# Performance work log

Measured on AMD Instinct MI355X. Metric: run time of the kernel, lower is better.

## Reference

```python
import jax, jax.numpy as jnp
import numpy as np

PRIMES = [2, 3, 5, 7]  # from prime2idx {"2":0,"3":1,"5":2,"7":3}
NEG = float('-inf')


def setup_inputs() -> dict:
    B, O, T, P, L = 16384, 7, 64, 4, 7
    ks = jax.random.split(jax.random.key(0), 12)
    return {
        'program_seq': jax.random.randint(ks[0], (B, 20), 0, 7),
        'order_mask': jnp.zeros((B, O), jnp.float32),
        'tile_remain_budgets': jax.random.randint(ks[1], (B, L, P), 0, T),
        'tile_masks': jnp.zeros((B, L, P, T), jnp.float32),
        'cur_buffer_level': 1,
        'loop_ind': 2,
        'remain_buffer_size': jax.random.uniform(ks[2], (B,), jnp.float32, 1.0, 1e6),
        'tile2_max': jax.random.randint(ks[3], (B,), 32, T),
        'max_temporal_tile2': jax.random.uniform(ks[4], (B,), jnp.float32, 0.0, 10.0),
        'sp_tile2_max': jax.random.randint(ks[5], (B,), 16, 32),
        'sp_tile2_min': jax.random.randint(ks[6], (B,), 0, 8),
        'order_logit': jax.random.normal(ks[7], (B, O), jnp.float32),
        'tile_logits': jax.random.normal(ks[8], (B, P, T), jnp.float32),
        'sp_tile2_logit': jax.random.normal(ks[9], (B, T), jnp.float32),
    }


def _sample(key, score, mask):
    # categorical sample, its log-prob, and the 'more-than-one-option' mask
    action = jax.random.categorical(key, score)
    lp = jnp.take_along_axis(jax.nn.log_softmax(score, axis=-1), action[:, None], axis=1)[:, 0]
    lpm = ((mask == 0).sum(axis=-1) > 1).astype(score.dtype)
    return action, lp, lpm


def reference(program_seq, order_mask, tile_remain_budgets, tile_masks,
              cur_buffer_level, loop_ind, remain_buffer_size, tile2_max,
              max_temporal_tile2, sp_tile2_max, sp_tile2_min,
              order_logit, tile_logits, sp_tile2_logit):
    B = program_seq.shape[0]
    T = tile_masks.shape[-1]
    P = tile_logits.shape[1]
    n_levels = 3  # len(buffer_size_list)
    keys = jax.random.split(jax.random.key(1), 2 + P)
    j = jnp.arange(T)[None, :]  # [1,T] position grid for range masks

    # ---- order head ----
    order_score = order_logit + order_mask
    order_action, order_lp, order_lpm = _sample(keys[0], order_score, order_mask)

    if cur_buffer_level == n_levels:
        log_probs = jnp.zeros((B, 1 + P + 1), order_score.dtype).at[:, 0].set(order_lp)
        log_prob_masks = jnp.zeros((B, 1 + P + 1), order_score.dtype).at[:, 0].set(order_lpm)
        return order_action, None, None, log_probs, log_prob_masks

    tile2_base = tile_masks[:, loop_ind, 0]  # [B,T]

    # ---- spatial tile2: vectorized [min,max] range mask (replaces per-sample loops) ----
    sp_mask = jnp.where((j > sp_tile2_max[:, None]) | (j < sp_tile2_min[:, None]), NEG, tile2_base)
    sp_score = sp_tile2_logit + sp_mask
    sp_action, sp_lp, sp_lpm = _sample(keys[1], sp_score, sp_mask)

    # ---- temporal tile2 ----
    tile2_min = sp_action
    t2_max = jnp.minimum(tile2_max, tile2_min + max_temporal_tile2.astype(tile2_max.dtype))
    t2_mask = jnp.where((j > t2_max[:, None]) | (j < tile2_min[:, None]), NEG, tile2_base)
    t2_score = tile_logits[:, 0] + t2_mask
    tile2_action, t2_lp, t2_lpm = _sample(keys[2], t2_score, t2_mask)

    tile_actions = [tile2_action]
    sp_tile_actions = [sp_action]
    log_probs = [order_lp, t2_lp]
    log_prob_masks = [order_lpm, t2_lpm]

    tile_action = tile2_action
    rbs = remain_buffer_size
    for p in range(1, P):  # small fixed loop over primes
        rbs = rbs / jnp.power(jnp.float32(PRIMES[p - 1]), tile_action.astype(jnp.float32))
        tmax = jnp.log2(jnp.clip(rbs, 1.0)) / np.log2(PRIMES[p])
        tmax = jnp.clip(tmax.astype(jnp.int32), 0, T - 1)
        tmax = jnp.minimum(tmax, tile_remain_budgets[:, loop_ind, p].astype(jnp.int32))
        mask = jnp.where(j > tmax[:, None], NEG, tile_masks[:, loop_ind, p])
        score = tile_logits[:, p] + mask
        tile_action, lp, lpm = _sample(keys[2 + p], score, mask)
        tile_actions.append(tile_action)
        log_probs.append(lp)
        log_prob_masks.append(lpm)
        sp_tile_actions.append(jnp.zeros((B,), program_seq.dtype))

    log_probs.append(sp_lp)
    log_prob_masks.append(sp_lpm)

    return (order_action,
            jnp.stack(tile_actions, axis=1),
            jnp.stack(sp_tile_actions, axis=1),
            jnp.stack(log_probs, axis=1),
            jnp.stack(log_prob_masks, axis=1))
```

## Files before the change

kernel.cpp:

```cpp
#include <hip/hip_runtime.h>
#include <stdint.h>
#include <math.h>

__host__ __device__ static inline void tf2x32(uint32_t k0, uint32_t k1,
                                              uint32_t& x0, uint32_t& x1) {
  uint32_t ks2 = k0 ^ k1 ^ 0x1BD11BDAu;
  x0 += k0; x1 += k1;
#define TFR(r) { x0 += x1; x1 = (x1 << (r)) | (x1 >> (32 - (r))); x1 ^= x0; }
  TFR(13) TFR(15) TFR(26) TFR(6)
  x0 += k1;  x1 += ks2 + 1u;
  TFR(17) TFR(29) TFR(16) TFR(24)
  x0 += ks2; x1 += k0 + 2u;
  TFR(13) TFR(15) TFR(26) TFR(6)
  x0 += k0;  x1 += k1 + 3u;
  TFR(17) TFR(29) TFR(16) TFR(24)
  x0 += k1;  x1 += ks2 + 4u;
  TFR(13) TFR(15) TFR(26) TFR(6)
  x0 += ks2; x1 += k0 + 5u;
#undef TFR
}

struct Keys { uint32_t k[12]; };

struct SampleOut { int action; float lp; float lpm; };

__device__ static inline SampleOut wave_sample(uint32_t k0, uint32_t k1,
                                               uint32_t flat_idx, int n, int t,
                                               float score, float maskval) {
  const bool active = (t < n);
  const float NEGINF = -__builtin_inff();
  float sc = active ? score : NEGINF;

  uint32_t x0 = 0u, x1 = flat_idx;
  tf2x32(k0, k1, x0, x1);
  uint32_t bits = x0 ^ x1;
  uint32_t fb = (bits >> 9) | 0x3f800000u;
  float f = __uint_as_float(fb) - 1.0f;
  const float tinyf = 1.1754943508222875e-38f;
  float u = fmaxf(tinyf, f + tinyf);
  float g = -logf(-logf(u));

  float z  = active ? (sc + g) : NEGINF;
  float es = active ? expf(sc) : 0.0f;

  float zv = z; int zi = t;
#pragma unroll
  for (int m = 1; m < 64; m <<= 1) {
    float ov = __shfl_xor(zv, m, 64);
    int   oi = __shfl_xor(zi, m, 64);
    es += __shfl_xor(es, m, 64);
    bool take = (ov > zv) || (ov == zv && oi < zi);
    zv = take ? ov : zv;
    zi = take ? oi : zi;
  }
  int action = zi;

  float sa = __shfl(sc, action, 64);
  float lp = sa - logf(es);

  unsigned long long ball = __ballot(active && (maskval == 0.0f));
  SampleOut r;
  r.action = action;
  r.lp = lp;
  r.lpm = (__popcll(ball) > 1) ? 1.0f : 0.0f;
  return r;
}

__device__ static inline double ipow_d(int base, int e) {
  double r = 1.0, b = (double)base;
  while (e) { if (e & 1) r *= b; b *= b; e >>= 1; }
  return r;
}

__global__ __launch_bounds__(256) void pt_kernel(
    const int*   __restrict__ loop_ind_p,
    const float* __restrict__ order_mask,
    const int*   __restrict__ tile_remain_budgets,
    const float* __restrict__ tile_masks,
    const float* __restrict__ remain_buffer_size,
    const int*   __restrict__ tile2_max,
    const float* __restrict__ max_temporal_tile2,
    const int*   __restrict__ sp_tile2_max,
    const int*   __restrict__ sp_tile2_min,
    const float* __restrict__ order_logit,
    const float* __restrict__ tile_logits,
    const float* __restrict__ sp_tile2_logit,
    float*       __restrict__ out,
    int B, int O, int T, int P, int L, Keys keys) {
  const int wave = threadIdx.x >> 6;
  const int t    = threadIdx.x & 63;
  const int b    = blockIdx.x * (blockDim.x >> 6) + wave;
  if (b >= B) return;

  const float NEGINF = -__builtin_inff();
  const int li = loop_ind_p[0];

  float om = (t < O) ? order_mask[(size_t)b * O + t] : 1.0f;
  float osc = (t < O) ? (order_logit[(size_t)b * O + t] + om) : NEGINF;
  SampleOut so = wave_sample(keys.k[0], keys.k[1],
                             (uint32_t)(b * O + t), O, t, osc, om);

  const float* tm_row = tile_masks + ((size_t)b * L + li) * P * T;
  float t2base = tm_row[t];
  int spmx = sp_tile2_max[b], spmn = sp_tile2_min[b];
  float spmask = (t > spmx || t < spmn) ? NEGINF : t2base;
  float spsc = sp_tile2_logit[(size_t)b * T + t] + spmask;
  SampleOut ssp = wave_sample(keys.k[2], keys.k[3],
                              (uint32_t)(b * T + t), T, t, spsc, spmask);

  int t2min = ssp.action;
  int mt = (int)max_temporal_tile2[b];
  int t2mx = min(tile2_max[b], t2min + mt);
  float t2mask = (t > t2mx || t < t2min) ? NEGINF : t2base;
  float t2sc = tile_logits[(size_t)b * P * T + t] + t2mask;
  SampleOut st2 = wave_sample(keys.k[4], keys.k[5],
                              (uint32_t)(b * T + t), T, t, t2sc, t2mask);

  const float L2P[4] = {1.0f, 1.5849625007211562f, 2.321928094887362f,
                        2.807354922057604f};
  const int PRIMES_[4] = {2, 3, 5, 7};
  int   pact[3];
  float plp[3], plpm[3];
  float rbs = remain_buffer_size[b];
  int prev = st2.action;
  for (int p = 1; p < P; ++p) {
    double pw = ipow_d(PRIMES_[p - 1], prev);
    rbs = (float)((double)rbs / pw);
    double v = log2(fmax((double)rbs, 1.0)) / (double)L2P[p];
    int tmax = (int)v;
    tmax = min(T - 1, max(0, tmax));
    tmax = min(tmax, tile_remain_budgets[((size_t)b * L + li) * P + p]);
    float mask = (t > tmax) ? NEGINF : tm_row[(size_t)p * T + t];
    float sc = tile_logits[((size_t)b * P + p) * T + t] + mask;
    SampleOut s = wave_sample(keys.k[2 * (2 + p)], keys.k[2 * (2 + p) + 1],
                              (uint32_t)(b * T + t), T, t, sc, mask);
    pact[p - 1] = s.action;
    plp[p - 1]  = s.lp;
    plpm[p - 1] = s.lpm;
    prev = s.action;
  }

  if (t == 0) {
    size_t Bz = (size_t)B;
    out[b] = (float)so.action;
    float* ta = out + Bz + (size_t)b * P;
    ta[0] = (float)st2.action;
    for (int p = 1; p < P; ++p) ta[p] = (float)pact[p - 1];
    float* sa = out + Bz * (1 + P) + (size_t)b * P;
    sa[0] = (float)ssp.action;
    for (int p = 1; p < P; ++p) sa[p] = 0.0f;
    int NL = 1 + P + 1;
    float* lp = out + Bz * (1 + 2 * P) + (size_t)b * NL;
    lp[0] = so.lp; lp[1] = st2.lp;
    for (int p = 1; p < P; ++p) lp[1 + p] = plp[p - 1];
    lp[NL - 1] = ssp.lp;
    float* lm = out + Bz * (1 + 2 * P + NL) + (size_t)b * NL;
    lm[0] = so.lpm; lm[1] = st2.lpm;
    for (int p = 1; p < P; ++p) lm[1 + p] = plpm[p - 1];
    lm[NL - 1] = ssp.lpm;
  }
}

extern "C" void kernel_launch(void* const* d_in, const int* in_sizes, int n_in,
                              void* d_out, int out_size, void* d_ws,
                              size_t ws_size, hipStream_t stream) {
  const int B = in_sizes[6];
  const int O = in_sizes[1] / B;
  const int T = in_sizes[13] / B;
  const int P = in_sizes[12] / (B * T);
  const int L = in_sizes[2] / (B * P);

  Keys keys;
  for (int j = 0; j < 6; ++j) {
    uint32_t x0 = 0u, x1 = (uint32_t)j;
    tf2x32(0u, 1u, x0, x1);
    keys.k[2 * j]     = x0;
    keys.k[2 * j + 1] = x1;
  }

  const int wavesPerBlock = 4;
  dim3 block(wavesPerBlock * 64);
  dim3 grid((B + wavesPerBlock - 1) / wavesPerBlock);
  pt_kernel<<<grid, block, 0, stream>>>(
      (const int*)d_in[5],
      (const float*)d_in[1],
      (const int*)d_in[2],
      (const float*)d_in[3],
      (const float*)d_in[6],
      (const int*)d_in[7],
      (const float*)d_in[8],
      (const int*)d_in[9],
      (const int*)d_in[10],
      (const float*)d_in[11],
      (const float*)d_in[12],
      (const float*)d_in[13],
      (float*)d_out, B, O, T, P, L, keys);
}
```

Baseline: 224.0 us.

## Precompute gumbel noise and scores upfront, use DPP wave reductions for sampling

```diff
diff --git a/kernel.cpp b/kernel.cpp
--- a/kernel.cpp
+++ b/kernel.cpp
@@ -24,13 +24,65 @@
 
 struct SampleOut { int action; float lp; float lpm; };
 
-__device__ static inline SampleOut wave_sample(uint32_t k0, uint32_t k1,
-                                               uint32_t flat_idx, int n, int t,
-                                               float score, float maskval) {
-  const bool active = (t < n);
-  const float NEGINF = -__builtin_inff();
-  float sc = active ? score : NEGINF;
-
+template <int CTRL>
+__device__ __forceinline__ float dpp_max_step(float v) {
+  int o = __builtin_amdgcn_update_dpp(__float_as_int(v), __float_as_int(v),
+                                      CTRL, 0xf, 0xf, false);
+  return fmaxf(v, __int_as_float(o));
+}
+template <int CTRL>
+__device__ __forceinline__ float dpp_add_step(float v) {
+  int o = __builtin_amdgcn_update_dpp(0, __float_as_int(v),
+                                      CTRL, 0xf, 0xf, false);
+  return v + __int_as_float(o);
+}
+__device__ __forceinline__ float wave_max_bcast(float v) {
+  v = dpp_max_step<0x111>(v);
+  v = dpp_max_step<0x112>(v);
+  v = dpp_max_step<0x114>(v);
+  v = dpp_max_step<0x118>(v);
+  v = dpp_max_step<0x142>(v);
+  v = dpp_max_step<0x143>(v);
+  return __int_as_float(__builtin_amdgcn_readlane(__float_as_int(v), 63));
+}
+__device__ __forceinline__ float wave_sum_bcast(float v) {
+  v = dpp_add_step<0x111>(v);
+  v = dpp_add_step<0x112>(v);
+  v = dpp_add_step<0x114>(v);
+  v = dpp_add_step<0x118>(v);
+  v = dpp_add_step<0x142>(v);
+  v = dpp_add_step<0x143>(v);
+  return __int_as_float(__builtin_amdgcn_readlane(__float_as_int(v), 63));
+}
+
+__device__ static inline SampleOut sample_pre(float z, float es, float sc_full,
+                                              bool lpm_pred) {
+  float zmax = wave_max_bcast(z);
+  unsigned long long ball = __ballot(z == zmax);
+  int action = __ffsll(ball) - 1;
+  float essum = wave_sum_bcast(es);
+  float sa = __int_as_float(
+      __builtin_amdgcn_readlane(__float_as_int(sc_full), action));
+  unsigned long long mb = __ballot(lpm_pred);
+  SampleOut r;
+  r.action = action;
+  r.lp = sa - logf(essum);
+  r.lpm = (__popcll(mb) > 1) ? 1.0f : 0.0f;
+  return r;
+}
+
+__device__ static inline double ipow_d(int base, int e) {
+  double r = 1.0, b = (double)base;
+#pragma unroll
+  for (int i = 0; i < 6; ++i) {
+    if (e & (1 << i)) r *= b;
+    b *= b;
+  }
+  return r;
+}
+
+__device__ static inline float gumbel_f(uint32_t k0, uint32_t k1,
+                                        uint32_t flat_idx) {
   uint32_t x0 = 0u, x1 = flat_idx;
   tf2x32(k0, k1, x0, x1);
   uint32_t bits = x0 ^ x1;
@@ -38,38 +90,7 @@
   float f = __uint_as_float(fb) - 1.0f;
   const float tinyf = 1.1754943508222875e-38f;
   float u = fmaxf(tinyf, f + tinyf);
-  float g = -logf(-logf(u));
-
-  float z  = active ? (sc + g) : NEGINF;
-  float es = active ? expf(sc) : 0.0f;
-
-  float zv = z; int zi = t;
-#pragma unroll
-  for (int m = 1; m < 64; m <<= 1) {
-    float ov = __shfl_xor(zv, m, 64);
-    int   oi = __shfl_xor(zi, m, 64);
-    es += __shfl_xor(es, m, 64);
-    bool take = (ov > zv) || (ov == zv && oi < zi);
-    zv = take ? ov : zv;
-    zi = take ? oi : zi;
-  }
-  int action = zi;
-
-  float sa = __shfl(sc, action, 64);
-  float lp = sa - logf(es);
-
-  unsigned long long ball = __ballot(active && (maskval == 0.0f));
-  SampleOut r;
-  r.action = action;
-  r.lp = lp;
-  r.lpm = (__popcll(ball) > 1) ? 1.0f : 0.0f;
-  return r;
-}
-
-__device__ static inline double ipow_d(int base, int e) {
-  double r = 1.0, b = (double)base;
-  while (e) { if (e & 1) r *= b; b *= b; e >>= 1; }
-  return r;
+  return -logf(-logf(u));
 }
 
 __global__ __launch_bounds__(256) void pt_kernel(
@@ -95,49 +116,88 @@
   const float NEGINF = -__builtin_inff();
   const int li = loop_ind_p[0];
 
-  float om = (t < O) ? order_mask[(size_t)b * O + t] : 1.0f;
+  float g0 = gumbel_f(keys.k[0],  keys.k[1],  (uint32_t)(b * O + t));
+  uint32_t fT = (uint32_t)(b * T + t);
+  float g1 = gumbel_f(keys.k[2],  keys.k[3],  fT);
+  float g2 = gumbel_f(keys.k[4],  keys.k[5],  fT);
+  float g3 = gumbel_f(keys.k[6],  keys.k[7],  fT);
+  float g4 = gumbel_f(keys.k[8],  keys.k[9],  fT);
+  float g5 = gumbel_f(keys.k[10], keys.k[11], fT);
+
+  float om  = (t < O) ? order_mask[(size_t)b * O + t] : 1.0f;
   float osc = (t < O) ? (order_logit[(size_t)b * O + t] + om) : NEGINF;
-  SampleOut so = wave_sample(keys.k[0], keys.k[1],
-                             (uint32_t)(b * O + t), O, t, osc, om);
 
   const float* tm_row = tile_masks + ((size_t)b * L + li) * P * T;
-  float t2base = tm_row[t];
+  const float* tl_row = tile_logits + (size_t)b * P * T;
+  float base0 = tm_row[t];
+  float base1 = tm_row[T + t];
+  float base2 = tm_row[2 * T + t];
+  float base3 = tm_row[3 * T + t];
+
   int spmx = sp_tile2_max[b], spmn = sp_tile2_min[b];
-  float spmask = (t > spmx || t < spmn) ? NEGINF : t2base;
-  float spsc = sp_tile2_logit[(size_t)b * T + t] + spmask;
-  SampleOut ssp = wave_sample(keys.k[2], keys.k[3],
-                              (uint32_t)(b * T + t), T, t, spsc, spmask);
+  float spmask = (t > spmx || t < spmn) ? NEGINF : base0;
+  float spsc   = sp_tile2_logit[(size_t)b * T + t] + spmask;
+
+  float sc2f = tl_row[t]         + base0;
+  float sc3f = tl_row[T + t]     + base1;
+  float sc4f = tl_row[2 * T + t] + base2;
+  float sc5f = tl_row[3 * T + t] + base3;
+  float es2f = expf(sc2f), es3f = expf(sc3f);
+  float es4f = expf(sc4f), es5f = expf(sc5f);
+  float z2f = sc2f + g2, z3f = sc3f + g3, z4f = sc4f + g4, z5f = sc5f + g5;
+
+  const int* budg = tile_remain_budgets + ((size_t)b * L + li) * P;
+
+  SampleOut so = sample_pre(osc + g0, expf(osc), osc,
+                            (t < O) && (om == 0.0f));
+
+  SampleOut ssp = sample_pre(spsc + g1, expf(spsc), spsc, spmask == 0.0f);
 
   int t2min = ssp.action;
   int mt = (int)max_temporal_tile2[b];
   int t2mx = min(tile2_max[b], t2min + mt);
-  float t2mask = (t > t2mx || t < t2min) ? NEGINF : t2base;
-  float t2sc = tile_logits[(size_t)b * P * T + t] + t2mask;
-  SampleOut st2 = wave_sample(keys.k[4], keys.k[5],
-                              (uint32_t)(b * T + t), T, t, t2sc, t2mask);
-
-  const float L2P[4] = {1.0f, 1.5849625007211562f, 2.321928094887362f,
-                        2.807354922057604f};
-  const int PRIMES_[4] = {2, 3, 5, 7};
+  bool pv2 = (t <= t2mx) && (t >= t2min);
+  SampleOut st2 = sample_pre(pv2 ? z2f : NEGINF, pv2 ? es2f : 0.0f, sc2f,
+                             pv2 && (base0 == 0.0f));
+
+  const float L2P1 = 1.5849625007211562f;
+  const float L2P2 = 2.321928094887362f;
+  const float L2P3 = 2.807354922057604f;
+
+  float rbs = remain_buffer_size[b];
   int   pact[3];
   float plp[3], plpm[3];
-  float rbs = remain_buffer_size[b];
+
   int prev = st2.action;
-  for (int p = 1; p < P; ++p) {
-    double pw = ipow_d(PRIMES_[p - 1], prev);
-    rbs = (float)((double)rbs / pw);
-    double v = log2(fmax((double)rbs, 1.0)) / (double)L2P[p];
-    int tmax = (int)v;
-    tmax = min(T - 1, max(0, tmax));
-    tmax = min(tmax, tile_remain_budgets[((size_t)b * L + li) * P + p]);
-    float mask = (t > tmax) ? NEGINF : tm_row[(size_t)p * T + t];
-    float sc = tile_logits[((size_t)b * P + p) * T + t] + mask;
-    SampleOut s = wave_sample(keys.k[2 * (2 + p)], keys.k[2 * (2 + p) + 1],
-                              (uint32_t)(b * T + t), T, t, sc, mask);
-    pact[p - 1] = s.action;
-    plp[p - 1]  = s.lp;
-    plpm[p - 1] = s.lpm;
-    prev = s.action;
+  {
+    rbs = (float)((double)rbs / ipow_d(2, prev));
+    double v = log2(fmax((double)rbs, 1.0)) / (double)L2P1;
+    int tmax = min(T - 1, max(0, (int)v));
+    tmax = min(tmax, budg[1]);
+    bool pv = (t <= tmax);
+    SampleOut s = sample_pre(pv ? z3f : NEGINF, pv ? es3f : 0.0f, sc3f,
+                             pv && (base1 == 0.0f));
+    pact[0] = s.action; plp[0] = s.lp; plpm[0] = s.lpm; prev = s.action;
+  }
+  {
+    rbs = (float)((double)rbs / ipow_d(3, prev));
+    double v = log2(fmax((double)rbs, 1.0)) / (double)L2P2;
+    int tmax = min(T - 1, max(0, (int)v));
+    tmax = min(tmax, budg[2]);
+    bool pv = (t <= tmax);
+    SampleOut s = sample_pre(pv ? z4f : NEGINF, pv ? es4f : 0.0f, sc4f,
+                             pv && (base2 == 0.0f));
+    pact[1] = s.action; plp[1] = s.lp; plpm[1] = s.lpm; prev = s.action;
+  }
+  {
+    rbs = (float)((double)rbs / ipow_d(5, prev));
+    double v = log2(fmax((double)rbs, 1.0)) / (double)L2P3;
+    int tmax = min(T - 1, max(0, (int)v));
+    tmax = min(tmax, budg[3]);
+    bool pv = (t <= tmax);
+    SampleOut s = sample_pre(pv ? z5f : NEGINF, pv ? es5f : 0.0f, sc5f,
+                             pv && (base3 == 0.0f));
+    pact[2] = s.action; plp[2] = s.lp; plpm[2] = s.lpm;
   }
 
   if (t == 0) {
@@ -145,19 +205,18 @@
     out[b] = (float)so.action;
     float* ta = out + Bz + (size_t)b * P;
     ta[0] = (float)st2.action;
-    for (int p = 1; p < P; ++p) ta[p] = (float)pact[p - 1];
+    ta[1] = (float)pact[0]; ta[2] = (float)pact[1]; ta[3] = (float)pact[2];
     float* sa = out + Bz * (1 + P) + (size_t)b * P;
-    sa[0] = (float)ssp.action;
-    for (int p = 1; p < P; ++p) sa[p] = 0.0f;
-    int NL = 1 + P + 1;
+    sa[0] = (float)ssp.action; sa[1] = 0.0f; sa[2] = 0.0f; sa[3] = 0.0f;
+    const int NL = 6;
     float* lp = out + Bz * (1 + 2 * P) + (size_t)b * NL;
     lp[0] = so.lp; lp[1] = st2.lp;
-    for (int p = 1; p < P; ++p) lp[1 + p] = plp[p - 1];
-    lp[NL - 1] = ssp.lp;
+    lp[2] = plp[0]; lp[3] = plp[1]; lp[4] = plp[2];
+    lp[5] = ssp.lp;
     float* lm = out + Bz * (1 + 2 * P + NL) + (size_t)b * NL;
     lm[0] = so.lpm; lm[1] = st2.lpm;
-    for (int p = 1; p < P; ++p) lm[1 + p] = plpm[p - 1];
-    lm[NL - 1] = ssp.lpm;
+    lm[2] = plpm[0]; lm[3] = plpm[1]; lm[4] = plpm[2];
+    lm[5] = ssp.lpm;
   }
 }
 
```

After: 214.6 us. 1.04x faster.
